# Kernel optimization log

Hardware: AMD Instinct MI355X
Metric: run time of the kernel (lower is better)

The kernel has to match this reference:

```python
import jax, jax.numpy as jnp
import numpy as np

BN_EPS = 1e-5


def setup_inputs() -> dict:
    key = jax.random.key(0)
    k1, k2 = jax.random.split(key)
    B, P, S, D = 8, 64, 256, 256
    x = jax.random.normal(k1, (B, P, S, D), dtype=jnp.float32)
    # kaiming_normal_ on (planes, S, S): std = sqrt(2 / fan_in), fan_in = S*S
    std = np.sqrt(2.0 / (S * S)).astype(np.float32)
    weights = jax.random.normal(k2, (P, S, S), dtype=jnp.float32) * std
    gamma = jnp.ones((P,), dtype=jnp.float32)
    beta = jnp.zeros((P,), dtype=jnp.float32)
    return {"x": x, "weights": weights, "gamma": gamma, "beta": beta}


def reference(x, weights, gamma, beta):
    # x: (B, P, S, D); weights: (P, S, S)
    D = x.shape[-1]
    inv_dim = 1.0 / jnp.sqrt(jnp.asarray(D, dtype=x.dtype))
    # scores: (B, P, S, S) = x @ x^T / sqrt(D)
    scores = jnp.einsum('bpsd,bptd->bpst', x, x) * inv_dim
    # weighted reduction over last axis -> (B, P, S, 1)
    red = jnp.sum(scores * weights[None], axis=-1, keepdims=True)
    y = x + red  # residual broadcast over D
    # BatchNorm2d in training mode: per-channel batch stats over (B, S, D)
    mean = jnp.mean(y, axis=(0, 2, 3), keepdims=True)
    var = jnp.var(y, axis=(0, 2, 3), keepdims=True)
    y_hat = (y - mean) * jax.lax.rsqrt(var + BN_EPS)
    return y_hat * gamma[None, :, None, None] + beta[None, :, None, None]
```

## Files before the change

### kernel.cpp

```cpp
#include <hip/hip_runtime.h>

typedef __attribute__((ext_vector_type(8))) short short8;
typedef __attribute__((ext_vector_type(4))) float f32x4;

#define NB 8
#define NP 64
#define NS 256
#define ND 256
#define LSTR 264

__device__ __forceinline__ unsigned short f2bf(float f) {
    unsigned int u = __float_as_uint(f);
    u = (u + 0x7FFFu + ((u >> 16) & 1u)) >> 16;
    return (unsigned short)u;
}

__global__ __launch_bounds__(256) void k0_wt(
    const float* __restrict__ w, float* __restrict__ wt)
{
    const int o  = blockIdx.x * 256 + threadIdx.x;
    const int c  = o & 15;
    const int jb = (o >> 4) & 3;
    const int ps = o >> 6;
    const float* row = w + (size_t)ps * NS + 64 * jb + c;
    f32x4 v;
    v.x = row[0]; v.y = row[16]; v.z = row[32]; v.w = row[48];
    reinterpret_cast<f32x4*>(wt)[o] = v;
}

__global__ __launch_bounds__(1024, 4) void k1_gemm_red(
    const float* __restrict__ x, const float* __restrict__ wt,
    float* __restrict__ red, float* __restrict__ Sx, float* __restrict__ Sxx)
{
    __shared__ unsigned short Xl[NS * LSTR];
    __shared__ float red_l[4][NS];

    const int t    = threadIdx.x;
    const int lane = t & 63;
    const int wv   = t >> 6;
    const int ib   = wv >> 2;
    const int jb   = wv & 3;
    const int p    = blockIdx.x & 63;
    const int b    = blockIdx.x >> 6;

    const float* xb      = x + (size_t)(b * NP + p) * (NS * ND);
    const size_t rowbase = (size_t)(b * NP + p) * NS;

    const int u   = lane >> 4;
    const int l16 = lane & 15;

    float a[4] = {0.f, 0.f, 0.f, 0.f};

    f32x4 acc[4][4] = {};

    auto STAGE = [&](int q) {
        #pragma unroll
        for (int j = 0; j < 4; ++j) {
            const int row = 16 * (4 * j + u) + wv;
            f32x4 v = *reinterpret_cast<const f32x4*>(
                xb + (size_t)row * ND + 64 * q + 4 * l16);
            float s = (v.x + v.y) + (v.z + v.w);
            #pragma unroll
            for (int off = 1; off < 16; off <<= 1) s += __shfl_xor(s, off, 64);
            a[j] += s;
            unsigned long long pk =
                  (unsigned long long)f2bf(v.x)
                | ((unsigned long long)f2bf(v.y) << 16)
                | ((unsigned long long)f2bf(v.z) << 32)
                | ((unsigned long long)f2bf(v.w) << 48);
            *reinterpret_cast<unsigned long long*>(
                &Xl[row * LSTR + 64 * q + 4 * l16]) = pk;
        }
    };

    auto GEMM = [&](int g) {
        #pragma unroll
        for (int kk = 0; kk < 2; ++kk) {
            const int kof = 64 * g + 32 * kk + u * 8;
            short8 afr[4], bfr[4];
            #pragma unroll
            for (int i = 0; i < 4; ++i)
                afr[i] = *reinterpret_cast<const short8*>(
                    &Xl[(64 * ib + 16 * i + l16) * LSTR + kof]);
            #pragma unroll
            for (int j = 0; j < 4; ++j)
                bfr[j] = *reinterpret_cast<const short8*>(
                    &Xl[(64 * jb + 16 * j + l16) * LSTR + kof]);
            #pragma unroll
            for (int i = 0; i < 4; ++i)
                #pragma unroll
                for (int j = 0; j < 4; ++j)
                    acc[i][j] = __builtin_amdgcn_mfma_f32_16x16x32_bf16(
                        afr[i], bfr[j], acc[i][j], 0, 0, 0);
        }
    };

    STAGE(0);
    __syncthreads();
    STAGE(1); GEMM(0);
    __syncthreads();
    STAGE(2); GEMM(1);
    __syncthreads();
    STAGE(3);
    if (l16 == 0) {
        #pragma unroll
        for (int j = 0; j < 4; ++j)
            Sx[rowbase + 16 * (4 * j + u) + wv] = a[j];
    }
    GEMM(2);
    __syncthreads();
    GEMM(3);

    const int qd = u;
    const int c  = l16;

    if (ib == jb && qd == (c >> 2)) {
        #pragma unroll
        for (int i = 0; i < 4; ++i)
            Sxx[rowbase + 64 * ib + 16 * i + c] = acc[i][i][c & 3];
    }

    const float* wtp = wt + (size_t)p * (NS * NS);
    #pragma unroll
    for (int i = 0; i < 4; ++i) {
        #pragma unroll
        for (int r = 0; r < 4; ++r) {
            const int rl = 16 * i + 4 * qd + r;
            const f32x4 wvec = *reinterpret_cast<const f32x4*>(
                wtp + (size_t)(64 * ib + rl) * NS + 64 * jb + 4 * c);
            float s = acc[i][0][r] * wvec.x + acc[i][1][r] * wvec.y
                    + acc[i][2][r] * wvec.z + acc[i][3][r] * wvec.w;
            #pragma unroll
            for (int off = 1; off < 16; off <<= 1)
                s += __shfl_xor(s, off, 64);
            if (c == 0) red_l[jb][64 * ib + rl] = s;
        }
    }
    __syncthreads();
    if (t < NS)
        red[rowbase + t] =
            (red_l[0][t] + red_l[1][t] + red_l[2][t] + red_l[3][t]) * 0.0625f;
}

__global__ __launch_bounds__(256) void k2_stats(
    const float* __restrict__ red, const float* __restrict__ Sx,
    const float* __restrict__ Sxx, const float* __restrict__ gamma,
    const float* __restrict__ beta, float* __restrict__ sb)
{
    __shared__ float l1[256], l2[256];
    const int p = blockIdx.x;
    const int t = threadIdx.x;
    float sy = 0.f, syy = 0.f;
    for (int n = t; n < NB * NS; n += 256) {
        int bb = n >> 8, s = n & 255;
        size_t idx = (size_t)(bb * NP + p) * NS + s;
        float r = red[idx], aa = Sx[idx], q = Sxx[idx];
        sy  += aa + 256.f * r;
        syy += q + 2.f * r * aa + 256.f * r * r;
    }
    l1[t] = sy; l2[t] = syy;
    __syncthreads();
    for (int off = 128; off > 0; off >>= 1) {
        if (t < off) { l1[t] += l1[t + off]; l2[t] += l2[t + off]; }
        __syncthreads();
    }
    if (t == 0) {
        const float invN = 1.f / (float)(NB * NS * ND);
        float mean = l1[0] * invN;
        float var  = l2[0] * invN - mean * mean;
        float sc   = gamma[p] * rsqrtf(var + 1e-5f);
        sb[p]      = sc;
        sb[64 + p] = beta[p] - mean * sc;
    }
}

__global__ __launch_bounds__(256) void k3_norm(
    const float* __restrict__ x, const float* __restrict__ red,
    const float* __restrict__ sb, float* __restrict__ out)
{
    const size_t f0 = (size_t)blockIdx.x * 1024 + threadIdx.x;
    #pragma unroll
    for (int k = 0; k < 4; ++k) {
        const size_t f = f0 + (size_t)k * 256;
        f32x4 v = reinterpret_cast<const f32x4*>(x)[f];
        const float r  = red[f >> 6];
        const int   pp = (int)((f >> 14) & 63);
        v = (v + r) * sb[pp] + sb[64 + pp];
        __builtin_nontemporal_store(v, reinterpret_cast<f32x4*>(out) + f);
    }
}

extern "C" void kernel_launch(void* const* d_in, const int* in_sizes, int n_in,
                              void* d_out, int out_size, void* d_ws, size_t ws_size,
                              hipStream_t stream)
{
    const float* x     = (const float*)d_in[0];
    const float* w     = (const float*)d_in[1];
    const float* gamma = (const float*)d_in[2];
    const float* beta  = (const float*)d_in[3];
    float* out = (float*)d_out;

    float* red = (float*)d_ws;
    float* Sx  = red + (size_t)NB * NP * NS;
    float* Sxx = Sx  + (size_t)NB * NP * NS;
    float* sb  = Sxx + (size_t)NB * NP * NS;
    float* wt  = sb + 128;

    hipLaunchKernelGGL(k0_wt, dim3((NP * NS * NS) / (4 * 256)), dim3(256), 0, stream,
                       w, wt);
    hipLaunchKernelGGL(k1_gemm_red, dim3(NB * NP), dim3(1024), 0, stream,
                       x, wt, red, Sx, Sxx);
    hipLaunchKernelGGL(k2_stats, dim3(NP), dim3(256), 0, stream,
                       red, Sx, Sxx, gamma, beta, sb);
    hipLaunchKernelGGL(k3_norm, dim3((NB * NP * NS * ND) / (16 * 256)), dim3(256),
                       0, stream, x, red, sb, out);
}
```

Measured before the change: 321.2 us.

## Drop weight transpose kernel, halve block to 8 waves with register-prefetched staging

Removes the separate weight-transpose kernel and reads the original weight layout directly with strided scalar loads in the reduction epilogue. The GEMM kernel now uses 512 threads, so each wave computes two 64x64 output tiles and shares its A fragments across both. Global loads for the next K-chunk are issued into registers before the current GEMM step and packed to LDS afterwards, so load latency overlaps the MFMA work. The costs are higher register pressure from the doubled accumulators plus the prefetch buffers, and less coalesced weight loads.

```diff
diff --git a/kernel.cpp b/kernel.cpp
--- a/kernel.cpp
+++ b/kernel.cpp
@@ -15,21 +15,8 @@
     return (unsigned short)u;
 }
 
-__global__ __launch_bounds__(256) void k0_wt(
-    const float* __restrict__ w, float* __restrict__ wt)
-{
-    const int o  = blockIdx.x * 256 + threadIdx.x;
-    const int c  = o & 15;
-    const int jb = (o >> 4) & 3;
-    const int ps = o >> 6;
-    const float* row = w + (size_t)ps * NS + 64 * jb + c;
-    f32x4 v;
-    v.x = row[0]; v.y = row[16]; v.z = row[32]; v.w = row[48];
-    reinterpret_cast<f32x4*>(wt)[o] = v;
-}
-
-__global__ __launch_bounds__(1024, 4) void k1_gemm_red(
-    const float* __restrict__ x, const float* __restrict__ wt,
+__global__ __launch_bounds__(512, 2) void k1_gemm_red(
+    const float* __restrict__ x, const float* __restrict__ w,
     float* __restrict__ red, float* __restrict__ Sx, float* __restrict__ Sxx)
 {
     __shared__ unsigned short Xl[NS * LSTR];
@@ -37,9 +24,9 @@
 
     const int t    = threadIdx.x;
     const int lane = t & 63;
-    const int wv   = t >> 6;
-    const int ib   = wv >> 2;
-    const int jb   = wv & 3;
+    const int wid  = t >> 6;
+    const int ib   = wid >> 1;
+    const int jb0  = 2 * (wid & 1);
     const int p    = blockIdx.x & 63;
     const int b    = blockIdx.x >> 6;
 
@@ -49,16 +36,23 @@
     const int u   = lane >> 4;
     const int l16 = lane & 15;
 
-    float a[4] = {0.f, 0.f, 0.f, 0.f};
-
-    f32x4 acc[4][4] = {};
-
-    auto STAGE = [&](int q) {
-        #pragma unroll
-        for (int j = 0; j < 4; ++j) {
-            const int row = 16 * (4 * j + u) + wv;
-            f32x4 v = *reinterpret_cast<const f32x4*>(
+    f32x4 ld[8];
+    float a[8] = {0,0,0,0,0,0,0,0};
+    f32x4 acc[2][4][4] = {};
+
+    auto ISSUE = [&](int q) {
+        #pragma unroll
+        for (int j = 0; j < 8; ++j) {
+            const int row = 32 * wid + 4 * j + u;
+            ld[j] = *reinterpret_cast<const f32x4*>(
                 xb + (size_t)row * ND + 64 * q + 4 * l16);
+        }
+    };
+    auto PACK = [&](int q) {
+        #pragma unroll
+        for (int j = 0; j < 8; ++j) {
+            const int row = 32 * wid + 4 * j + u;
+            f32x4 v = ld[j];
             float s = (v.x + v.y) + (v.z + v.w);
             #pragma unroll
             for (int off = 1; off < 16; off <<= 1) s += __shfl_xor(s, off, 64);
@@ -72,68 +66,75 @@
                 &Xl[row * LSTR + 64 * q + 4 * l16]) = pk;
         }
     };
-
     auto GEMM = [&](int g) {
         #pragma unroll
         for (int kk = 0; kk < 2; ++kk) {
             const int kof = 64 * g + 32 * kk + u * 8;
-            short8 afr[4], bfr[4];
+            short8 afr[4];
             #pragma unroll
             for (int i = 0; i < 4; ++i)
                 afr[i] = *reinterpret_cast<const short8*>(
                     &Xl[(64 * ib + 16 * i + l16) * LSTR + kof]);
             #pragma unroll
-            for (int j = 0; j < 4; ++j)
-                bfr[j] = *reinterpret_cast<const short8*>(
-                    &Xl[(64 * jb + 16 * j + l16) * LSTR + kof]);
-            #pragma unroll
-            for (int i = 0; i < 4; ++i)
+            for (int tt = 0; tt < 2; ++tt) {
+                short8 bfr[4];
                 #pragma unroll
                 for (int j = 0; j < 4; ++j)
-                    acc[i][j] = __builtin_amdgcn_mfma_f32_16x16x32_bf16(
-                        afr[i], bfr[j], acc[i][j], 0, 0, 0);
+                    bfr[j] = *reinterpret_cast<const short8*>(
+                        &Xl[(64 * (jb0 + tt) + 16 * j + l16) * LSTR + kof]);
+                #pragma unroll
+                for (int i = 0; i < 4; ++i)
+                    #pragma unroll
+                    for (int j = 0; j < 4; ++j)
+                        acc[tt][i][j] = __builtin_amdgcn_mfma_f32_16x16x32_bf16(
+                            afr[i], bfr[j], acc[tt][i][j], 0, 0, 0);
+            }
         }
     };
 
-    STAGE(0);
-    __syncthreads();
-    STAGE(1); GEMM(0);
-    __syncthreads();
-    STAGE(2); GEMM(1);
-    __syncthreads();
-    STAGE(3);
+    ISSUE(0); PACK(0);
+    __syncthreads();
+    ISSUE(1); GEMM(0); PACK(1);
+    __syncthreads();
+    ISSUE(2); GEMM(1); PACK(2);
+    __syncthreads();
+    ISSUE(3); GEMM(2); PACK(3);
     if (l16 == 0) {
         #pragma unroll
-        for (int j = 0; j < 4; ++j)
-            Sx[rowbase + 16 * (4 * j + u) + wv] = a[j];
-    }
-    GEMM(2);
+        for (int j = 0; j < 8; ++j)
+            Sx[rowbase + 32 * wid + 4 * j + u] = a[j];
+    }
     __syncthreads();
     GEMM(3);
 
-    const int qd = u;
-    const int c  = l16;
-
-    if (ib == jb && qd == (c >> 2)) {
-        #pragma unroll
-        for (int i = 0; i < 4; ++i)
-            Sxx[rowbase + 64 * ib + 16 * i + c] = acc[i][i][c & 3];
-    }
-
-    const float* wtp = wt + (size_t)p * (NS * NS);
     #pragma unroll
-    for (int i = 0; i < 4; ++i) {
-        #pragma unroll
-        for (int r = 0; r < 4; ++r) {
-            const int rl = 16 * i + 4 * qd + r;
-            const f32x4 wvec = *reinterpret_cast<const f32x4*>(
-                wtp + (size_t)(64 * ib + rl) * NS + 64 * jb + 4 * c);
-            float s = acc[i][0][r] * wvec.x + acc[i][1][r] * wvec.y
-                    + acc[i][2][r] * wvec.z + acc[i][3][r] * wvec.w;
-            #pragma unroll
-            for (int off = 1; off < 16; off <<= 1)
-                s += __shfl_xor(s, off, 64);
-            if (c == 0) red_l[jb][64 * ib + rl] = s;
+    for (int tt = 0; tt < 2; ++tt) {
+        if (ib == jb0 + tt && u == (l16 >> 2)) {
+            #pragma unroll
+            for (int i = 0; i < 4; ++i)
+                Sxx[rowbase + 64 * ib + 16 * i + l16] = acc[tt][i][i][l16 & 3];
+        }
+    }
+
+    const float* wp = w + (size_t)p * (NS * NS);
+    #pragma unroll
+    for (int tt = 0; tt < 2; ++tt) {
+        const int jb = jb0 + tt;
+        #pragma unroll
+        for (int i = 0; i < 4; ++i) {
+            #pragma unroll
+            for (int r = 0; r < 4; ++r) {
+                const int rl = 16 * i + 4 * u + r;
+                const float* wrow = wp + (size_t)(64 * ib + rl) * NS + 64 * jb + l16;
+                float s = acc[tt][i][0][r] * wrow[0]
+                        + acc[tt][i][1][r] * wrow[16]
+                        + acc[tt][i][2][r] * wrow[32]
+                        + acc[tt][i][3][r] * wrow[48];
+                #pragma unroll
+                for (int off = 1; off < 16; off <<= 1)
+                    s += __shfl_xor(s, off, 64);
+                if (l16 == 0) red_l[jb][64 * ib + rl] = s;
+            }
         }
     }
     __syncthreads();
@@ -204,12 +205,9 @@
     float* Sx  = red + (size_t)NB * NP * NS;
     float* Sxx = Sx  + (size_t)NB * NP * NS;
     float* sb  = Sxx + (size_t)NB * NP * NS;
-    float* wt  = sb + 128;
-
-    hipLaunchKernelGGL(k0_wt, dim3((NP * NS * NS) / (4 * 256)), dim3(256), 0, stream,
-                       w, wt);
-    hipLaunchKernelGGL(k1_gemm_red, dim3(NB * NP), dim3(1024), 0, stream,
-                       x, wt, red, Sx, Sxx);
+
+    hipLaunchKernelGGL(k1_gemm_red, dim3(NB * NP), dim3(512), 0, stream,
+                       x, w, red, Sx, Sxx);
     hipLaunchKernelGGL(k2_stats, dim3(NP), dim3(256), 0, stream,
                        red, Sx, Sxx, gamma, beta, sb);
     hipLaunchKernelGGL(k3_norm, dim3((NB * NP * NS * ND) / (16 * 256)), dim3(256),
```

After: 315.3 us. Within noise of the previous version (-1.8%).
